# Kernel optimization log

Measured on AMD Instinct MI355X. Metric: run time of the kernel, lower is better.

The kernel has to match this reference:

```python
import jax, jax.numpy as jnp
import numpy as np

D_MODEL = 1024
NUM_HEADS = 16
HEAD_DIM = D_MODEL // NUM_HEADS
B, T = 4, 2048


def setup_inputs() -> dict:
    key = jax.random.key(0)
    ks = jax.random.split(key, 6)
    s = 1.0 / np.sqrt(D_MODEL)  # ~ nn.Linear init scale
    return {
        "x_q": jax.random.normal(ks[0], (B, T, D_MODEL), jnp.float32),
        "x_kv": jax.random.normal(ks[1], (B, T, D_MODEL), jnp.float32),
        "Wq": jax.random.uniform(ks[2], (D_MODEL, D_MODEL), jnp.float32, -s, s),
        "Wk": jax.random.uniform(ks[3], (D_MODEL, D_MODEL), jnp.float32, -s, s),
        "Wv": jax.random.uniform(ks[4], (D_MODEL, D_MODEL), jnp.float32, -s, s),
        "Wo": jax.random.uniform(ks[5], (D_MODEL, D_MODEL), jnp.float32, -s, s),
    }


def reference(x_q, x_kv, Wq, Wk, Wv, Wo):
    Bq, Tq, C = x_q.shape
    Tk = x_kv.shape[1]
    # torch nn.Linear: y = x @ W.T
    q = (x_q @ Wq.T).reshape(Bq, Tq, NUM_HEADS, HEAD_DIM).transpose(0, 2, 1, 3)
    k = (x_kv @ Wk.T).reshape(Bq, Tk, NUM_HEADS, HEAD_DIM).transpose(0, 2, 1, 3)
    v = (x_kv @ Wv.T).reshape(Bq, Tk, NUM_HEADS, HEAD_DIM).transpose(0, 2, 1, 3)
    scores = jnp.einsum("bhqd,bhkd->bhqk", q, k) / jnp.sqrt(
        jnp.asarray(HEAD_DIM, x_q.dtype)
    )
    causal = jnp.triu(jnp.ones((Tq, Tk), bool), k=1)  # True above diagonal
    scores = jnp.where(causal, -jnp.inf, scores)
    attn = jax.nn.softmax(scores, axis=-1)
    out = jnp.einsum("bhqk,bhkd->bhqd", attn, v)
    out = out.transpose(0, 2, 1, 3).reshape(Bq, Tq, C)
    return out @ Wo.T
```

## Files before the change

### kernel.cpp

```cpp
#include <hip/hip_runtime.h>
#include <stdint.h>

#define T_SEQ 2048
#define NH 16
#define HD 64
#define DM 1024
#define BB 4
#define MROWS (BB * T_SEQ)

typedef __attribute__((ext_vector_type(8))) __bf16 bf16x8;
typedef __attribute__((ext_vector_type(8))) unsigned short u16x8;
typedef __attribute__((ext_vector_type(4))) unsigned short u16x4;
typedef __attribute__((ext_vector_type(4))) float f32x4;

__device__ __forceinline__ unsigned short f2bf(float f) {
  return __builtin_bit_cast(unsigned short, (__bf16)f);
}

__device__ __forceinline__ bf16x8 ld8_f32(const float* __restrict__ p) {
  f32x4 a = *(const f32x4*)p;
  f32x4 b = *(const f32x4*)(p + 4);
  u16x8 u;
#pragma unroll
  for (int i = 0; i < 4; ++i) {
    u[i]     = f2bf(a[i]);
    u[i + 4] = f2bf(b[i]);
  }
  return __builtin_bit_cast(bf16x8, u);
}

__device__ __forceinline__ bf16x8 ld8_bf(const unsigned short* p) {
  return __builtin_bit_cast(bf16x8, *(const u16x8*)p);
}

__device__ __forceinline__ bf16x8 ld8_lds(const unsigned short* p) {
  u16x4 a = *(const u16x4*)p;
  u16x4 b = *(const u16x4*)(p + 4);
  return __builtin_bit_cast(bf16x8,
      __builtin_shufflevector(a, b, 0, 1, 2, 3, 4, 5, 6, 7));
}

__device__ __forceinline__ u16x4 lo4(u16x8 v) {
  return __builtin_shufflevector(v, v, 0, 1, 2, 3);
}
__device__ __forceinline__ u16x4 hi4(u16x8 v) {
  return __builtin_shufflevector(v, v, 4, 5, 6, 7);
}

__device__ __forceinline__ void gload_lds16(const unsigned short* g,
                                            unsigned short* l) {
  __builtin_amdgcn_global_load_lds(
      (const __attribute__((address_space(1))) unsigned int*)g,
      (__attribute__((address_space(3))) unsigned int*)l, 16, 0, 0);
}

__global__ __launch_bounds__(256) void conv_f32_bf16(
    const float* __restrict__ src, unsigned short* __restrict__ dst, int n8) {
  const int i = blockIdx.x * 256 + threadIdx.x;
  if (i < n8)
    *(u16x8*)(dst + (size_t)i * 8) =
        __builtin_bit_cast(u16x8, ld8_f32(src + (size_t)i * 8));
}

__global__ __launch_bounds__(256) void conv_w4(
    const float* __restrict__ s0, const float* __restrict__ s1,
    const float* __restrict__ s2, const float* __restrict__ s3,
    unsigned short* __restrict__ d012, unsigned short* __restrict__ d3,
    int n8) {
  const int y = blockIdx.y;
  const float* src = (y == 0) ? s0 : (y == 1) ? s1 : (y == 2) ? s2 : s3;
  unsigned short* dst = (y < 3) ? d012 + (size_t)y * DM * DM : d3;
  const int i = blockIdx.x * 256 + threadIdx.x;
  if (i < n8)
    *(u16x8*)(dst + (size_t)i * 8) =
        __builtin_bit_cast(u16x8, ld8_f32(src + (size_t)i * 8));
}

template <int MODE>
__global__ __launch_bounds__(256) void gemm128(
    const unsigned short* __restrict__ A, const unsigned short* __restrict__ B,
    void* __restrict__ Cv, void* __restrict__ Cv2, int M, int N, int K) {
  __shared__ __align__(16) unsigned short As[2][128 * 32];
  __shared__ __align__(16) unsigned short Bs[2][128 * 32];

  const int t = threadIdx.x;
  const int lane = t & 63, wave = t >> 6;
  const int lin = (int)(blockIdx.x + gridDim.x * blockIdx.y);
  const int nx = N >> 7;
  const int mpx = (M >> 7) >> 3;
  const int xcd = lin & 7, slot = lin >> 3;
  const int m0 = (xcd * mpx + slot / nx) * 128;
  const int n0 = (slot % nx) * 128;

  const int srow = t >> 2;
  const int scol = (t & 3) * 8;
  const unsigned short* ga0 = A + (size_t)(m0 + srow) * K + scol;
  const unsigned short* ga1 = A + (size_t)(m0 + 64 + srow) * K + scol;
  const unsigned short* gb0 = B + (size_t)(n0 + srow) * K + scol;
  const unsigned short* gb1 = B + (size_t)(n0 + 64 + srow) * K + scol;
  const int lo0 = (wave * 16) * 32, lo1 = (64 + wave * 16) * 32;

  const int mw = (wave >> 1) * 64, nw = (wave & 1) * 64;
  const int fr = lane & 15, fq = (lane >> 4) * 8;

  f32x4 acc[4][4];
#pragma unroll
  for (int i = 0; i < 4; ++i)
#pragma unroll
    for (int j = 0; j < 4; ++j) acc[i][j] = (f32x4){0.f, 0.f, 0.f, 0.f};

  for (int k0 = 0; k0 < K; k0 += 64) {
    __syncthreads();
    gload_lds16(ga0 + k0, &As[0][lo0]);
    gload_lds16(ga1 + k0, &As[0][lo1]);
    gload_lds16(gb0 + k0, &Bs[0][lo0]);
    gload_lds16(gb1 + k0, &Bs[0][lo1]);
    gload_lds16(ga0 + k0 + 32, &As[1][lo0]);
    gload_lds16(ga1 + k0 + 32, &As[1][lo1]);
    gload_lds16(gb0 + k0 + 32, &Bs[1][lo0]);
    gload_lds16(gb1 + k0 + 32, &Bs[1][lo1]);
    __syncthreads();

#pragma unroll
    for (int ks = 0; ks < 2; ++ks) {
      bf16x8 af[4], bfr[4];
#pragma unroll
      for (int i = 0; i < 4; ++i)
        af[i] = ld8_bf(&As[ks][(mw + i * 16 + fr) * 32 + fq]);
#pragma unroll
      for (int j = 0; j < 4; ++j)
        bfr[j] = ld8_bf(&Bs[ks][(nw + j * 16 + fr) * 32 + fq]);
#pragma unroll
      for (int i = 0; i < 4; ++i)
#pragma unroll
        for (int j = 0; j < 4; ++j)
          acc[i][j] = __builtin_amdgcn_mfma_f32_16x16x32_bf16(
              af[i], bfr[j], acc[i][j], 0, 0, 0);
    }
  }

  const int orow = (lane >> 4) * 4, ocol = lane & 15;
  const bool kv_lo = (MODE == 3) && (n0 < DM);
#pragma unroll
  for (int i = 0; i < 4; ++i)
#pragma unroll
    for (int j = 0; j < 4; ++j) {
      if constexpr (MODE == 2) {
        const int mb = m0 + mw + i * 16 + orow;
        const int n = n0 + nw + j * 16 + ocol;
        u16x4 pk;
#pragma unroll
        for (int r = 0; r < 4; ++r) pk[r] = f2bf(acc[i][j][r]);
        unsigned short* dst = (unsigned short*)Cv +
            ((size_t)((mb >> 11) * NH + (n >> 6)) * HD + (n & 63)) * T_SEQ +
            (mb & 2047);
        *(u16x4*)dst = pk;
      } else if constexpr (MODE == 3) {
        const int mb = m0 + mw + i * 16 + orow;
        const int n = n0 + nw + j * 16 + ocol;
        if (kv_lo) {
#pragma unroll
          for (int r = 0; r < 4; ++r)
            ((unsigned short*)Cv)[(size_t)(mb + r) * DM + n] =
                f2bf(acc[i][j][r]);
        } else {
          const int nv = n - DM;
          u16x4 pk;
#pragma unroll
          for (int r = 0; r < 4; ++r) pk[r] = f2bf(acc[i][j][r]);
          unsigned short* dst = (unsigned short*)Cv2 +
              ((size_t)((mb >> 11) * NH + (nv >> 6)) * HD + (nv & 63)) *
                  T_SEQ +
              (mb & 2047);
          *(u16x4*)dst = pk;
        }
      } else {
#pragma unroll
        for (int r = 0; r < 4; ++r) {
          const size_t idx = (size_t)(m0 + mw + i * 16 + orow + r) * N +
                             (n0 + nw + j * 16 + ocol);
          if constexpr (MODE == 1)
            ((float*)Cv)[idx] = acc[i][j][r];
          else
            ((unsigned short*)Cv)[idx] = f2bf(acc[i][j][r]);
        }
      }
    }
}

#define ASTR 68

__global__ __launch_bounds__(256, 2) void attn_flash2(
    const unsigned short* Qw, const unsigned short* __restrict__ Kw,
    const unsigned short* __restrict__ Vt, unsigned short* Ow) {
  __shared__ __align__(16) unsigned short k_lds[2][64][ASTR];
  __shared__ __align__(16) unsigned short vt_lds[2][64][ASTR];
  __shared__ __align__(16) unsigned short p_lds[4][32][ASTR];
  __shared__ float alpha_lds[4][32];
  __shared__ float l_lds[4][32];

  const int tid = threadIdx.x, lane = tid & 63, wave = tid >> 6;
  const int c16 = lane & 15, quad = lane >> 4;
  const int b = blockIdx.z, h = blockIdx.y;
  const int pi = blockIdx.x;
  const int qb0A = (15 - pi) * 128;
  const int qb0B = pi * 128;
  const size_t rkbase = (size_t)b * T_SEQ * DM + (size_t)h * HD;
  const size_t vtbase = (size_t)(b * NH + h) * HD * T_SEQ;

  const int q_loA = qb0A + wave * 32;
  const int q_loB = qb0B + wave * 32;

  bf16x8 qfA[2][2], qfB[2][2];
#pragma unroll
  for (int nf = 0; nf < 2; ++nf) {
    const unsigned short* qpA =
        Qw + rkbase + (size_t)(q_loA + nf * 16 + c16) * DM + quad * 8;
    qfA[nf][0] = ld8_bf(qpA);
    qfA[nf][1] = ld8_bf(qpA + 32);
    const unsigned short* qpB =
        Qw + rkbase + (size_t)(q_loB + nf * 16 + c16) * DM + quad * 8;
    qfB[nf][0] = ld8_bf(qpB);
    qfB[nf][1] = ld8_bf(qpB + 32);
  }

  f32x4 oA[2][4], oB[2][4];
#pragma unroll
  for (int nf = 0; nf < 2; ++nf)
#pragma unroll
    for (int j = 0; j < 4; ++j) {
      oA[nf][j] = (f32x4){0.f, 0.f, 0.f, 0.f};
      oB[nf][j] = (f32x4){0.f, 0.f, 0.f, 0.f};
    }
  float mA[2] = {-3.0e38f, -3.0e38f}, lA[2] = {0.f, 0.f};
  float mB[2] = {-3.0e38f, -3.0e38f}, lB[2] = {0.f, 0.f};

  const int srow = tid >> 2;
  const int scol = (tid & 3) * 16;
  const int ntiles = (qb0A + 191) >> 6;
  const int ntA_w = (q_loA + 95) >> 6;
  const int ntB_w = (q_loB + 95) >> 6;

  const unsigned short* kp0 = Kw + rkbase + (size_t)srow * DM + scol;
  const unsigned short* vp0 = Vt + vtbase + (size_t)srow * T_SEQ + scol;

  auto subtile = [&](const bf16x8 (&qf)[2][2], f32x4 (&o)[2][4],
                     float (&m_r)[2], float (&l_r)[2], const int q_lo,
                     const int kb0, const int bi) {
    f32x4 s[4][2];
    __builtin_amdgcn_s_setprio(1);
#pragma unroll
    for (int mf = 0; mf < 4; ++mf) {
      const unsigned short* kr = &k_lds[bi][mf * 16 + c16][quad * 8];
      const bf16x8 k0 = ld8_lds(kr);
      const bf16x8 k1 = ld8_lds(kr + 32);
#pragma unroll
      for (int nf = 0; nf < 2; ++nf) {
        f32x4 a = {0.f, 0.f, 0.f, 0.f};
        a = __builtin_amdgcn_mfma_f32_16x16x32_bf16(k0, qf[nf][0], a, 0, 0, 0);
        a = __builtin_amdgcn_mfma_f32_16x16x32_bf16(k1, qf[nf][1], a, 0, 0, 0);
        s[mf][nf] = a;
      }
    }
    __builtin_amdgcn_s_setprio(0);
    if (kb0 + 63 > q_lo) {
#pragma unroll
      for (int mf = 0; mf < 4; ++mf) {
        const int key0 = kb0 + mf * 16 + quad * 4;
#pragma unroll
        for (int nf = 0; nf < 2; ++nf) {
          const int qg = q_lo + nf * 16 + c16;
#pragma unroll
          for (int r = 0; r < 4; ++r)
            s[mf][nf][r] =
                (key0 + r <= qg) ? s[mf][nf][r] * 0.125f : -3.0e38f;
        }
      }
    } else {
#pragma unroll
      for (int mf = 0; mf < 4; ++mf)
#pragma unroll
        for (int nf = 0; nf < 2; ++nf)
#pragma unroll
          for (int r = 0; r < 4; ++r) s[mf][nf][r] *= 0.125f;
    }

#pragma unroll
    for (int nf = 0; nf < 2; ++nf) {
      float mx = -3.0e38f;
#pragma unroll
      for (int mf = 0; mf < 4; ++mf)
#pragma unroll
        for (int r = 0; r < 4; ++r) mx = fmaxf(mx, s[mf][nf][r]);
      mx = fmaxf(mx, __shfl_xor(mx, 16, 64));
      mx = fmaxf(mx, __shfl_xor(mx, 32, 64));
      const float m_new = fmaxf(m_r[nf], mx);
      const float al = __expf(m_r[nf] - m_new);
      m_r[nf] = m_new;
      float ps = 0.f;
#pragma unroll
      for (int mf = 0; mf < 4; ++mf) {
        u16x4 pk;
#pragma unroll
        for (int r = 0; r < 4; ++r) {
          const float e = __expf(s[mf][nf][r] - m_new);
          ps += e;
          pk[r] = f2bf(e);
        }
        *(u16x4*)&p_lds[wave][nf * 16 + c16][mf * 16 + quad * 4] = pk;
      }
      ps += __shfl_xor(ps, 16, 64);
      ps += __shfl_xor(ps, 32, 64);
      l_r[nf] = l_r[nf] * al + ps;
      if (quad == 0) alpha_lds[wave][nf * 16 + c16] = al;
    }
    __threadfence_block();

#pragma unroll
    for (int nf = 0; nf < 2; ++nf) {
      float alr[4];
#pragma unroll
      for (int r = 0; r < 4; ++r)
        alr[r] = alpha_lds[wave][nf * 16 + quad * 4 + r];
#pragma unroll
      for (int j = 0; j < 4; ++j)
#pragma unroll
        for (int r = 0; r < 4; ++r) o[nf][j][r] *= alr[r];
    }

    bf16x8 pf[2][2];
#pragma unroll
    for (int nf = 0; nf < 2; ++nf) {
      const unsigned short* pw = &p_lds[wave][nf * 16 + c16][quad * 8];
      pf[nf][0] = ld8_lds(pw);
      pf[nf][1] = ld8_lds(pw + 32);
    }
    __builtin_amdgcn_s_setprio(1);
#pragma unroll
    for (int j = 0; j < 4; ++j) {
      const unsigned short* vr = &vt_lds[bi][j * 16 + c16][quad * 8];
      const bf16x8 v0 = ld8_lds(vr);
      const bf16x8 v1 = ld8_lds(vr + 32);
#pragma unroll
      for (int nf = 0; nf < 2; ++nf) {
        o[nf][j] = __builtin_amdgcn_mfma_f32_16x16x32_bf16(pf[nf][0], v0,
                                                           o[nf][j], 0, 0, 0);
        o[nf][j] = __builtin_amdgcn_mfma_f32_16x16x32_bf16(pf[nf][1], v1,
                                                           o[nf][j], 0, 0, 0);
      }
    }
    __builtin_amdgcn_s_setprio(0);
  };

  {
    u16x8 ka = *(const u16x8*)kp0;
    u16x8 kc = *(const u16x8*)(kp0 + 8);
    u16x8 va = *(const u16x8*)vp0;
    u16x8 vc = *(const u16x8*)(vp0 + 8);
    *(u16x4*)&k_lds[0][srow][scol]       = lo4(ka);
    *(u16x4*)&k_lds[0][srow][scol + 4]   = hi4(ka);
    *(u16x4*)&k_lds[0][srow][scol + 8]   = lo4(kc);
    *(u16x4*)&k_lds[0][srow][scol + 12]  = hi4(kc);
    *(u16x4*)&vt_lds[0][srow][scol]      = lo4(va);
    *(u16x4*)&vt_lds[0][srow][scol + 4]  = hi4(va);
    *(u16x4*)&vt_lds[0][srow][scol + 8]  = lo4(vc);
    *(u16x4*)&vt_lds[0][srow][scol + 12] = hi4(vc);
  }
  __syncthreads();

  int cur = 0;
  for (int t = 0; t < ntiles; ++t) {
    const int kb0 = t * 64;
    const bool pf = (t + 1 < ntiles);
    u16x8 ka, kc, va, vc;
    if (pf) {
      const unsigned short* kp = kp0 + (size_t)(kb0 + 64) * DM;
      ka = *(const u16x8*)kp;
      kc = *(const u16x8*)(kp + 8);
      const unsigned short* vp = vp0 + (kb0 + 64);
      va = *(const u16x8*)vp;
      vc = *(const u16x8*)(vp + 8);
    }
    if (t < ntA_w) subtile(qfA, oA, mA, lA, q_loA, kb0, cur);
    if (t < ntB_w) subtile(qfB, oB, mB, lB, q_loB, kb0, cur);
    if (pf) {
      const int nb = cur ^ 1;
      *(u16x4*)&k_lds[nb][srow][scol]       = lo4(ka);
      *(u16x4*)&k_lds[nb][srow][scol + 4]   = hi4(ka);
      *(u16x4*)&k_lds[nb][srow][scol + 8]   = lo4(kc);
      *(u16x4*)&k_lds[nb][srow][scol + 12]  = hi4(kc);
      *(u16x4*)&vt_lds[nb][srow][scol]      = lo4(va);
      *(u16x4*)&vt_lds[nb][srow][scol + 4]  = hi4(va);
      *(u16x4*)&vt_lds[nb][srow][scol + 8]  = lo4(vc);
      *(u16x4*)&vt_lds[nb][srow][scol + 12] = hi4(vc);
      __syncthreads();
      cur = nb;
    }
  }

  auto epi = [&](f32x4 (&o)[2][4], float (&l_r)[2], const int q_lo) {
    if (quad == 0) {
      l_lds[wave][c16] = l_r[0];
      l_lds[wave][16 + c16] = l_r[1];
    }
    __threadfence_block();
#pragma unroll
    for (int nf = 0; nf < 2; ++nf)
#pragma unroll
      for (int r = 0; r < 4; ++r) {
        const int qg = q_lo + nf * 16 + quad * 4 + r;
        const float inv = 1.0f / l_lds[wave][nf * 16 + quad * 4 + r];
        unsigned short* orow = Ow + rkbase + (size_t)qg * DM;
#pragma unroll
        for (int j = 0; j < 4; ++j)
          orow[j * 16 + c16] = f2bf(o[nf][j][r] * inv);
      }
  };
  epi(oA, lA, q_loA);
  __threadfence_block();
  epi(oB, lB, q_loB);
}

extern "C" void kernel_launch(void* const* d_in, const int* in_sizes, int n_in,
                              void* d_out, int out_size, void* d_ws, size_t ws_size,
                              hipStream_t stream) {
  const float* x_q  = (const float*)d_in[0];
  const float* x_kv = (const float*)d_in[1];
  const float* Wq   = (const float*)d_in[2];
  const float* Wk   = (const float*)d_in[3];
  const float* Wv   = (const float*)d_in[4];
  const float* Wo   = (const float*)d_in[5];
  float* out = (float*)d_out;

  unsigned short* scr  = (unsigned short*)d_out;
  unsigned short* Sx   = scr;
  unsigned short* Wk_b = scr + (size_t)MROWS * DM;
  unsigned short* Wv_b = Wk_b + (size_t)DM * DM;
  unsigned short* Wq_b = Wv_b + (size_t)DM * DM;

  unsigned short* qb   = (unsigned short*)d_ws;
  unsigned short* kb   = qb + (size_t)MROWS * DM;
  unsigned short* vtb  = kb + (size_t)MROWS * DM;
  unsigned short* Wo_b = vtb + (size_t)MROWS * DM;

  const int nW8 = DM * DM / 8;
  const int nX8 = MROWS * DM / 8;

  conv_w4<<<dim3(nW8 / 256, 4), 256, 0, stream>>>(Wk, Wv, Wq, Wo, Wk_b, Wo_b,
                                                  nW8);
  conv_f32_bf16<<<nX8 / 256, 256, 0, stream>>>(x_kv, Sx, nX8);

  gemm128<3><<<dim3(2 * DM / 128, MROWS / 128), 256, 0, stream>>>(
      Sx, Wk_b, kb, vtb, MROWS, 2 * DM, DM);
  conv_f32_bf16<<<nX8 / 256, 256, 0, stream>>>(x_q, Sx, nX8);
  gemm128<0><<<dim3(DM / 128, MROWS / 128), 256, 0, stream>>>(
      Sx, Wq_b, qb, nullptr, MROWS, DM, DM);
  attn_flash2<<<dim3(8, NH, BB), 256, 0, stream>>>(qb, kb, vtb, qb);
  gemm128<1><<<dim3(DM / 128, MROWS / 128), 256, 0, stream>>>(
      qb, Wo_b, out, nullptr, MROWS, DM, DM);
}
```

Before: 302.9 us.

## Double-buffer LDS tiles in gemm128 to overlap global loads with MFMA

The gemm128 kernel now keeps two LDS buffers per operand. It issues the asynchronous global-to-LDS loads for the next K tile before computing on the current one, so memory latency can hide behind the MFMA work. This also drops the leading barrier in each iteration, leaving one barrier per tile. The cost is twice the shared memory per block, which may lower occupancy.

```diff
diff --git a/kernel.cpp b/kernel.cpp
--- a/kernel.cpp
+++ b/kernel.cpp
@@ -80,8 +80,8 @@
 __global__ __launch_bounds__(256) void gemm128(
     const unsigned short* __restrict__ A, const unsigned short* __restrict__ B,
     void* __restrict__ Cv, void* __restrict__ Cv2, int M, int N, int K) {
-  __shared__ __align__(16) unsigned short As[2][128 * 32];
-  __shared__ __align__(16) unsigned short Bs[2][128 * 32];
+  __shared__ __align__(16) unsigned short As[2][2][128 * 32];
+  __shared__ __align__(16) unsigned short Bs[2][2][128 * 32];
 
   const int t = threadIdx.x;
   const int lane = t & 63, wave = t >> 6;
@@ -109,27 +109,33 @@
 #pragma unroll
     for (int j = 0; j < 4; ++j) acc[i][j] = (f32x4){0.f, 0.f, 0.f, 0.f};
 
-  for (int k0 = 0; k0 < K; k0 += 64) {
-    __syncthreads();
-    gload_lds16(ga0 + k0, &As[0][lo0]);
-    gload_lds16(ga1 + k0, &As[0][lo1]);
-    gload_lds16(gb0 + k0, &Bs[0][lo0]);
-    gload_lds16(gb1 + k0, &Bs[0][lo1]);
-    gload_lds16(ga0 + k0 + 32, &As[1][lo0]);
-    gload_lds16(ga1 + k0 + 32, &As[1][lo1]);
-    gload_lds16(gb0 + k0 + 32, &Bs[1][lo0]);
-    gload_lds16(gb1 + k0 + 32, &Bs[1][lo1]);
-    __syncthreads();
-
+  auto stage = [&](int buf, int k0) {
+    gload_lds16(ga0 + k0,      &As[buf][0][lo0]);
+    gload_lds16(ga1 + k0,      &As[buf][0][lo1]);
+    gload_lds16(gb0 + k0,      &Bs[buf][0][lo0]);
+    gload_lds16(gb1 + k0,      &Bs[buf][0][lo1]);
+    gload_lds16(ga0 + k0 + 32, &As[buf][1][lo0]);
+    gload_lds16(ga1 + k0 + 32, &As[buf][1][lo1]);
+    gload_lds16(gb0 + k0 + 32, &Bs[buf][1][lo0]);
+    gload_lds16(gb1 + k0 + 32, &Bs[buf][1][lo1]);
+  };
+
+  stage(0, 0);
+  __syncthreads();
+
+  const int NT = K >> 6;
+  int cur = 0;
+  for (int kt = 0; kt < NT; ++kt) {
+    if (kt + 1 < NT) stage(cur ^ 1, (kt + 1) << 6);
 #pragma unroll
     for (int ks = 0; ks < 2; ++ks) {
       bf16x8 af[4], bfr[4];
 #pragma unroll
       for (int i = 0; i < 4; ++i)
-        af[i] = ld8_bf(&As[ks][(mw + i * 16 + fr) * 32 + fq]);
+        af[i] = ld8_bf(&As[cur][ks][(mw + i * 16 + fr) * 32 + fq]);
 #pragma unroll
       for (int j = 0; j < 4; ++j)
-        bfr[j] = ld8_bf(&Bs[ks][(nw + j * 16 + fr) * 32 + fq]);
+        bfr[j] = ld8_bf(&Bs[cur][ks][(nw + j * 16 + fr) * 32 + fq]);
 #pragma unroll
       for (int i = 0; i < 4; ++i)
 #pragma unroll
@@ -137,6 +143,8 @@
           acc[i][j] = __builtin_amdgcn_mfma_f32_16x16x32_bf16(
               af[i], bfr[j], acc[i][j], 0, 0, 0);
     }
+    __syncthreads();
+    cur ^= 1;
   }
 
   const int orow = (lane >> 4) * 4, ocol = lane & 15;
```

Measured after the change: 295.8 us. 2.4% less time.
